# Kernel tuning notes

Measured on AMD Instinct MI355X. Metric: run time of the kernel, lower is better.

## Reference

```python
import jax, jax.numpy as jnp
import numpy as np

B, D = 8192, 128
TEMP = 0.07
EPS = 1e-12  # F.normalize default eps (clamp on norm)


def _l2norm(x):
    n = jnp.sqrt(jnp.sum(x * x, axis=1, keepdims=True))
    return x / jnp.maximum(n, EPS)


def setup_inputs() -> dict:
    key = jax.random.key(0)
    k1, k2, k3, k4 = jax.random.split(key, 4)
    return {
        "feat_fv": jax.random.normal(k1, (B, D), dtype=jnp.float32),
        "feat_fi": jax.random.normal(k2, (B, D), dtype=jnp.float32),
        "feat_v": jax.random.normal(k3, (B, D), dtype=jnp.float32),
        "feat_i": jax.random.normal(k4, (B, D), dtype=jnp.float32),
    }


def reference(feat_fv, feat_fi, feat_v, feat_i):
    fv = _l2norm(feat_fv)
    fi = _l2norm(feat_fi)
    v = _l2norm(feat_v)
    vi = _l2norm(feat_i)

    # positive logits: per-sample dot products [B]
    pos_v = jnp.sum(fv * v, axis=1)
    pos_i = jnp.sum(fi * vi, axis=1)
    use_v = pos_v >= pos_i                      # branch condition per row
    pos = jnp.where(use_v, pos_v, pos_i)        # [B]

    # full pairwise dot products, branch-select per row
    Sv = jnp.einsum('bd,kd->bk', fv, v)         # [B, B]
    Si = jnp.einsum('bd,kd->bk', fi, vi)        # [B, B]
    S = jnp.where(use_v[:, None], Sv, Si)       # [B, B]

    n = S.shape[0]
    diag = jnp.eye(n, dtype=bool)
    # negatives exclude the positive (diagonal) entry -> mask to -inf
    neg_logits = jnp.where(diag, -jnp.inf, S / TEMP)  # [B, B]

    # cross-entropy with target class 0 (the positive), reduction='none':
    # loss_b = logsumexp([pos/T, negs/T]) - pos/T
    lse = jnp.logaddexp(pos / TEMP, jax.scipy.special.logsumexp(neg_logits, axis=1))
    return lse - pos / TEMP
```

## Files before the change

kernel.cpp:

```cpp
#include <hip/hip_runtime.h>
#include <math.h>

#define Bsz 8192
#define Dd  128
#define BM  64
#define NSLICE 16
#define NTILE  (512 / NSLICE / 4)
#define ROT2(x) ((((x) << 2) | ((x) >> 4)) & 63)

typedef __attribute__((ext_vector_type(8))) short short8;
typedef __attribute__((ext_vector_type(4))) float float4v;

static constexpr float INV_T = 1.0f / 0.07f;
static constexpr float K1 =  20.60992915555662f;
static constexpr float K2 = -20.60992915555662f;
static constexpr float SCALE     = 1099511627776.0f;
static constexpr float INV_SCALE = 1.0f / 1099511627776.0f;
#define CNT_SHIFT 55
#define NCONTRIB  (NSLICE * 4)
#define SUM_MASK  ((1ULL << CNT_SHIFT) - 1ULL)

static __device__ inline unsigned pack_bf16(float x, float y) {
    union { float f; unsigned u; } a, b;
    a.f = x; b.f = y;
    unsigned ra = a.u + 0x7FFF + ((a.u >> 16) & 1);
    unsigned rb = b.u + 0x7FFF + ((b.u >> 16) & 1);
    return (ra >> 16) | (rb & 0xFFFF0000u);
}

__global__ void init_kernel(unsigned long long* __restrict__ cnt) {
    if (threadIdx.x == 0) cnt[0] = 0ull;
}

__global__ __launch_bounds__(1024) void prep_kernel(
    const float4* __restrict__ fv4, const float4* __restrict__ fi4,
    const float4* __restrict__ v4,  const float4* __restrict__ vi4,
    unsigned* __restrict__ Xb, uint2* __restrict__ Yf0, uint2* __restrict__ Yf1,
    float* __restrict__ posArr, int* __restrict__ origArr, int* __restrict__ flagArr,
    unsigned long long* __restrict__ lAcc64, unsigned long long* __restrict__ cnt)
{
    __shared__ unsigned sT0[32 * 66];
    __shared__ unsigned sT1[32 * 66];
    __shared__ int sFlagL[32];
    __shared__ int sRank[32];
    __shared__ unsigned sBase[2];

    const int t    = threadIdx.x;
    const int wave = t >> 6;
    const int lane = t & 63;
    const int half = lane >> 5;
    const int c    = lane & 31;
    const int rl   = wave * 2 + half;
    const int b    = blockIdx.x * 32 + rl;
    const int src  = b * 32 + c;

    const float4 afv = fv4[src];
    const float4 afi = fi4[src];
    const float4 av  = v4[src];
    const float4 avi = vi4[src];

    float nfv = afv.x*afv.x + afv.y*afv.y + afv.z*afv.z + afv.w*afv.w;
    float nfi = afi.x*afi.x + afi.y*afi.y + afi.z*afi.z + afi.w*afi.w;
    float nv  = av.x*av.x   + av.y*av.y   + av.z*av.z   + av.w*av.w;
    float nvi = avi.x*avi.x + avi.y*avi.y + avi.z*avi.z + avi.w*avi.w;
    float dv  = afv.x*av.x  + afv.y*av.y  + afv.z*av.z  + afv.w*av.w;
    float di  = afi.x*avi.x + afi.y*avi.y + afi.z*avi.z + afi.w*avi.w;

    #pragma unroll
    for (int m = 1; m < 32; m <<= 1) {
        nfv += __shfl_xor(nfv, m);
        nfi += __shfl_xor(nfi, m);
        nv  += __shfl_xor(nv,  m);
        nvi += __shfl_xor(nvi, m);
        dv  += __shfl_xor(dv,  m);
        di  += __shfl_xor(di,  m);
    }

    const float rnfv = 1.0f / fmaxf(sqrtf(nfv), 1e-12f);
    const float rnfi = 1.0f / fmaxf(sqrtf(nfi), 1e-12f);
    const float rnv  = 1.0f / fmaxf(sqrtf(nv ), 1e-12f);
    const float rnvi = 1.0f / fmaxf(sqrtf(nvi), 1e-12f);

    const float pos_v = dv * rnfv * rnv;
    const float pos_i = di * rnfi * rnvi;
    const bool useV = (pos_v >= pos_i);
    const float pos = useV ? pos_v : pos_i;

    uint2 w0y = make_uint2(pack_bf16(av.x  * rnv,  av.y  * rnv),
                           pack_bf16(av.z  * rnv,  av.w  * rnv));
    uint2 w1y = make_uint2(pack_bf16(avi.x * rnvi, avi.y * rnvi),
                           pack_bf16(avi.z * rnvi, avi.w * rnvi));
    *(uint2*)&sT0[rl * 66 + c * 2] = w0y;
    *(uint2*)&sT1[rl * 66 + c * 2] = w1y;
    if (c == 0) sFlagL[rl] = useV ? 0 : 1;
    __syncthreads();

    if (t < 64) {
        const int f = (lane < 32) ? sFlagL[lane] : 2;
        const unsigned long long m0 = __ballot(f == 0);
        const unsigned long long m1 = __ballot(f == 1);
        if (lane == 0) {
            const unsigned long long add =
                (unsigned long long)__popcll(m0) | ((unsigned long long)__popcll(m1) << 32);
            const unsigned long long ret = atomicAdd(cnt, add);
            sBase[0] = (unsigned)(ret & 0xffffffffull);
            sBase[1] = (unsigned)(ret >> 32);
        }
        if (lane < 32) {
            const unsigned long long below = (1ull << lane) - 1ull;
            sRank[lane] = (f == 0) ? (int)__popcll(m0 & below) : (int)__popcll(m1 & below);
        }
    }

    {
        const int tl = t >> 9;
        const int kc = (t >> 7) & 3;
        const int lp = (t >> 1) & 63;
        const int w0 = (t & 1) * 2;
        const int row = tl * 16 + (lp & 15);
        const int s   = kc * 16 + (lp >> 4) * 4 + w0;
        Yf0[blockIdx.x * 1024 + t] = *(const uint2*)&sT0[row * 66 + s];
        Yf1[blockIdx.x * 1024 + t] = *(const uint2*)&sT1[row * 66 + s];
    }
    __syncthreads();

    const int f  = sFlagL[rl];
    const int rk = sRank[rl];
    const int p  = (f == 0) ? (int)(sBase[0] + rk) : (Bsz - 1 - (int)(sBase[1] + rk));

    const float sc = useV ? rnfv : rnfi;
    const float x0 = useV ? afv.x : afi.x;
    const float x1 = useV ? afv.y : afi.y;
    const float x2 = useV ? afv.z : afi.z;
    const float x3 = useV ? afv.w : afi.w;
    ((uint2*)Xb)[p * 32 + c] = make_uint2(pack_bf16(x0 * sc, x1 * sc),
                                          pack_bf16(x2 * sc, x3 * sc));

    if (c == 0) {
        posArr[p]  = pos;
        origArr[p] = b;
        flagArr[p] = f;
        lAcc64[p]  = 0ull;
    }
}

__global__ __launch_bounds__(256, 4) void main_kernel(
    const unsigned short* __restrict__ Xb,
    const uint4* __restrict__ Yf0q, const uint4* __restrict__ Yf1q,
    const int* __restrict__ flagArr, unsigned long long* __restrict__ lAcc64,
    const float* __restrict__ posArr, const int* __restrict__ origArr,
    float* __restrict__ out)
{
    __shared__ uint4 sXf[1024];
    __shared__ int sFlag[BM];
    __shared__ int sHas[2];

    const int t    = threadIdx.x;
    const int wave = t >> 6;
    const int lane = t & 63;
    const int quad = lane >> 4;
    const int mrow = lane & 15;
    const int slice = blockIdx.x & (NSLICE - 1);
    const int p0    = (blockIdx.x >> 4) * BM;

    if (t < 2) sHas[t] = 0;
    __syncthreads();
    if (t < BM) {
        const int f = flagArr[p0 + t];
        sFlag[t] = f;
        atomicOr(&sHas[f], 1);
    }

    #pragma unroll
    for (int it = 0; it < 4; ++it) {
        const int i = t + it * 256;
        const int row = i >> 4, ch = i & 15;
        const uint4 val = ((const uint4*)Xb)[(p0 + row) * 16 + ch];
        const int blk16 = (row >> 4) * 4 + (ch >> 2);
        const int slot  = (ch & 3) * 16 + (row & 15);
        sXf[blk16 * 64 + ROT2(slot)] = val;
    }
    __syncthreads();

    short8 afr[4][4];
    #pragma unroll
    for (int rt = 0; rt < 4; ++rt)
        #pragma unroll
        for (int kc = 0; kc < 4; ++kc)
            afr[rt][kc] = *(const short8*)&sXf[(rt * 4 + kc) * 64 + ROT2(lane)];

    const int g0 = slice * (NTILE * 4) + wave * NTILE;

    for (int phase = 0; phase < 2; ++phase) {
        if (!sHas[phase]) continue;
        const uint4* __restrict__ yb = (phase ? Yf1q : Yf0q) + (size_t)g0 * 256 + lane;

        float rowsum[4][4] = {};

        short8 b0 = *(const short8*)&yb[0];
        short8 b1 = *(const short8*)&yb[64];
        short8 b2 = *(const short8*)&yb[128];
        short8 b3 = *(const short8*)&yb[192];

        #pragma unroll 1
        for (int jt = 0; jt < NTILE; ++jt) {
            float4v acc[4] = {};
            #pragma unroll
            for (int rt = 0; rt < 4; ++rt)
                acc[rt] = __builtin_amdgcn_mfma_f32_16x16x32_bf16(afr[rt][0], b0, acc[rt], 0, 0, 0);
            #pragma unroll
            for (int rt = 0; rt < 4; ++rt)
                acc[rt] = __builtin_amdgcn_mfma_f32_16x16x32_bf16(afr[rt][1], b1, acc[rt], 0, 0, 0);
            if (jt < NTILE - 1) {
                b0 = *(const short8*)&yb[256];
                b1 = *(const short8*)&yb[320];
            }
            #pragma unroll
            for (int rt = 0; rt < 4; ++rt)
                acc[rt] = __builtin_amdgcn_mfma_f32_16x16x32_bf16(afr[rt][2], b2, acc[rt], 0, 0, 0);
            #pragma unroll
            for (int rt = 0; rt < 4; ++rt)
                acc[rt] = __builtin_amdgcn_mfma_f32_16x16x32_bf16(afr[rt][3], b3, acc[rt], 0, 0, 0);
            if (jt < NTILE - 1) {
                b2 = *(const short8*)&yb[384];
                b3 = *(const short8*)&yb[448];
            }
            yb += 256;

            #pragma unroll
            for (int rt = 0; rt < 4; ++rt)
                #pragma unroll
                for (int r = 0; r < 4; ++r)
                    rowsum[rt][r] += exp2f(fmaf(acc[rt][r], K1, K2));
        }

        #pragma unroll
        for (int m = 1; m < 16; m <<= 1)
            #pragma unroll
            for (int rt = 0; rt < 4; ++rt)
                #pragma unroll
                for (int r = 0; r < 4; ++r)
                    rowsum[rt][r] += __shfl_xor(rowsum[rt][r], m);

        if (mrow == 0) {
            #pragma unroll
            for (int rt = 0; rt < 4; ++rt)
                #pragma unroll
                for (int r = 0; r < 4; ++r) {
                    const int row = rt * 16 + quad * 4 + r;
                    if (sFlag[row] == phase) {
                        const unsigned long long add =
                            (unsigned long long)(rowsum[rt][r] * SCALE)
                            | (1ULL << CNT_SHIFT);
                        const unsigned long long ret =
                            atomicAdd(&lAcc64[p0 + row], add);
                        if ((ret >> CNT_SHIFT) == NCONTRIB - 1) {
                            const unsigned long long tot = (ret + add) & SUM_MASK;
                            const float s = (float)tot * INV_SCALE;
                            out[origArr[p0 + row]] =
                                logf(s) + INV_T - posArr[p0 + row] * INV_T;
                        }
                    }
                }
        }
    }
}

extern "C" void kernel_launch(void* const* d_in, const int* in_sizes, int n_in,
                              void* d_out, int out_size, void* d_ws, size_t ws_size,
                              hipStream_t stream)
{
    const float4* fv = (const float4*)d_in[0];
    const float4* fi = (const float4*)d_in[1];
    const float4* v  = (const float4*)d_in[2];
    const float4* vi = (const float4*)d_in[3];
    float* out = (float*)d_out;

    unsigned short* Xb  = (unsigned short*)d_ws;
    unsigned short* Yf0 = Xb  + Bsz * Dd;
    unsigned short* Yf1 = Yf0 + Bsz * Dd;
    float* posArr = (float*)(Yf1 + Bsz * Dd);
    unsigned long long* lAcc64 =
        (unsigned long long*)(posArr + Bsz);
    int*  origArr = (int*)(lAcc64 + Bsz);
    int*  flagArr = origArr + Bsz;
    unsigned long long* cnt = (unsigned long long*)(flagArr + Bsz);

    hipLaunchKernelGGL(init_kernel, dim3(1), dim3(64), 0, stream, cnt);
    hipLaunchKernelGGL(prep_kernel, dim3(Bsz / 32), dim3(1024), 0, stream,
                       fv, fi, v, vi, (unsigned*)Xb, (uint2*)Yf0, (uint2*)Yf1,
                       posArr, origArr, flagArr, lAcc64, cnt);
    hipLaunchKernelGGL(main_kernel, dim3((Bsz / BM) * NSLICE), dim3(256), 0, stream,
                       Xb, (const uint4*)Yf0, (const uint4*)Yf1, flagArr, lAcc64,
                       posArr, origArr, out);
}
```

Before: 130.9 us.

## Software-pipeline exp with MFMA via double accumulators, halve slices, drop LDS staging

The tile loop now keeps two accumulator sets, so the exp2 row-sum work for the previous tile is interleaved with the MFMAs for the current tile. The aim is to hide transcendental latency behind matrix ops. A fragments are now loaded directly from global memory in MFMA layout instead of being staged through rotated shared memory, which removes one barrier and the LDS traffic. Flag presence is computed with wave ballots instead of shared atomics. NSLICE drops from 16 to 8, which doubles the tiles per wave and halves the number of blocks and atomic contributions per row, at the cost of less parallelism and more registers.

```diff
diff --git a/kernel.cpp b/kernel.cpp
--- a/kernel.cpp
+++ b/kernel.cpp
@@ -4,9 +4,8 @@
 #define Bsz 8192
 #define Dd  128
 #define BM  64
-#define NSLICE 16
+#define NSLICE 8
 #define NTILE  (512 / NSLICE / 4)
-#define ROT2(x) ((((x) << 2) | ((x) >> 4)) & 63)
 
 typedef __attribute__((ext_vector_type(8))) short short8;
 typedef __attribute__((ext_vector_type(4))) float float4v;
@@ -151,7 +150,6 @@
     const float* __restrict__ posArr, const int* __restrict__ origArr,
     float* __restrict__ out)
 {
-    __shared__ uint4 sXf[1024];
     __shared__ int sFlag[BM];
     __shared__ int sHas[2];
 
@@ -161,78 +159,79 @@
     const int quad = lane >> 4;
     const int mrow = lane & 15;
     const int slice = blockIdx.x & (NSLICE - 1);
-    const int p0    = (blockIdx.x >> 4) * BM;
-
-    if (t < 2) sHas[t] = 0;
-    __syncthreads();
-    if (t < BM) {
-        const int f = flagArr[p0 + t];
-        sFlag[t] = f;
-        atomicOr(&sHas[f], 1);
-    }
-
-    #pragma unroll
-    for (int it = 0; it < 4; ++it) {
-        const int i = t + it * 256;
-        const int row = i >> 4, ch = i & 15;
-        const uint4 val = ((const uint4*)Xb)[(p0 + row) * 16 + ch];
-        const int blk16 = (row >> 4) * 4 + (ch >> 2);
-        const int slot  = (ch & 3) * 16 + (row & 15);
-        sXf[blk16 * 64 + ROT2(slot)] = val;
-    }
-    __syncthreads();
+    const int p0    = (blockIdx.x >> 3) * BM;
 
     short8 afr[4][4];
     #pragma unroll
     for (int rt = 0; rt < 4; ++rt)
         #pragma unroll
         for (int kc = 0; kc < 4; ++kc)
-            afr[rt][kc] = *(const short8*)&sXf[(rt * 4 + kc) * 64 + ROT2(lane)];
+            afr[rt][kc] = *(const short8*)&Xb[(size_t)(p0 + rt * 16 + mrow) * 128
+                                              + kc * 32 + quad * 8];
+
+    if (t < 64) {
+        const int f = flagArr[p0 + t];
+        sFlag[t] = f;
+        const unsigned long long m0 = __ballot(f == 0);
+        const unsigned long long m1 = __ballot(f == 1);
+        if (t == 0) { sHas[0] = (m0 != 0ull); sHas[1] = (m1 != 0ull); }
+    }
+    __syncthreads();
 
     const int g0 = slice * (NTILE * 4) + wave * NTILE;
+
+#define MFMA4(ACC, KC, BB)                                                         \
+    _Pragma("unroll")                                                              \
+    for (int rt = 0; rt < 4; ++rt)                                                 \
+        ACC[rt] = __builtin_amdgcn_mfma_f32_16x16x32_bf16(afr[rt][KC], BB, ACC[rt], 0, 0, 0);
+
+#define EXPQ(P, RT)                                                                \
+    _Pragma("unroll")                                                              \
+    for (int r = 0; r < 4; ++r)                                                    \
+        rowsum[RT][r] += exp2f(fmaf(P[RT][r], K1, K2));
+
+#define STEP(ACC, PACC, PF) do {                                                   \
+        ACC[0] = (float4v){0.f,0.f,0.f,0.f}; ACC[1] = (float4v){0.f,0.f,0.f,0.f};  \
+        ACC[2] = (float4v){0.f,0.f,0.f,0.f}; ACC[3] = (float4v){0.f,0.f,0.f,0.f};  \
+        MFMA4(ACC, 0, b0); MFMA4(ACC, 1, b1);                                      \
+        EXPQ(PACC, 0); EXPQ(PACC, 1);                                              \
+        if (PF) { b0 = *(const short8*)&yb[256]; b1 = *(const short8*)&yb[320]; }  \
+        MFMA4(ACC, 2, b2); MFMA4(ACC, 3, b3);                                      \
+        EXPQ(PACC, 2); EXPQ(PACC, 3);                                              \
+        if (PF) { b2 = *(const short8*)&yb[384]; b3 = *(const short8*)&yb[448]; }  \
+        yb += 256;                                                                 \
+    } while (0)
+
+#define STEP0(ACC, PF) do {                                                        \
+        ACC[0] = (float4v){0.f,0.f,0.f,0.f}; ACC[1] = (float4v){0.f,0.f,0.f,0.f};  \
+        ACC[2] = (float4v){0.f,0.f,0.f,0.f}; ACC[3] = (float4v){0.f,0.f,0.f,0.f};  \
+        MFMA4(ACC, 0, b0); MFMA4(ACC, 1, b1);                                      \
+        if (PF) { b0 = *(const short8*)&yb[256]; b1 = *(const short8*)&yb[320]; }  \
+        MFMA4(ACC, 2, b2); MFMA4(ACC, 3, b3);                                      \
+        if (PF) { b2 = *(const short8*)&yb[384]; b3 = *(const short8*)&yb[448]; }  \
+        yb += 256;                                                                 \
+    } while (0)
 
     for (int phase = 0; phase < 2; ++phase) {
         if (!sHas[phase]) continue;
         const uint4* __restrict__ yb = (phase ? Yf1q : Yf0q) + (size_t)g0 * 256 + lane;
 
         float rowsum[4][4] = {};
+        float4v accA[4], accB[4];
 
         short8 b0 = *(const short8*)&yb[0];
         short8 b1 = *(const short8*)&yb[64];
         short8 b2 = *(const short8*)&yb[128];
         short8 b3 = *(const short8*)&yb[192];
 
+        STEP0(accA, 1);
         #pragma unroll 1
-        for (int jt = 0; jt < NTILE; ++jt) {
-            float4v acc[4] = {};
-            #pragma unroll
-            for (int rt = 0; rt < 4; ++rt)
-                acc[rt] = __builtin_amdgcn_mfma_f32_16x16x32_bf16(afr[rt][0], b0, acc[rt], 0, 0, 0);
-            #pragma unroll
-            for (int rt = 0; rt < 4; ++rt)
-                acc[rt] = __builtin_amdgcn_mfma_f32_16x16x32_bf16(afr[rt][1], b1, acc[rt], 0, 0, 0);
-            if (jt < NTILE - 1) {
-                b0 = *(const short8*)&yb[256];
-                b1 = *(const short8*)&yb[320];
-            }
-            #pragma unroll
-            for (int rt = 0; rt < 4; ++rt)
-                acc[rt] = __builtin_amdgcn_mfma_f32_16x16x32_bf16(afr[rt][2], b2, acc[rt], 0, 0, 0);
-            #pragma unroll
-            for (int rt = 0; rt < 4; ++rt)
-                acc[rt] = __builtin_amdgcn_mfma_f32_16x16x32_bf16(afr[rt][3], b3, acc[rt], 0, 0, 0);
-            if (jt < NTILE - 1) {
-                b2 = *(const short8*)&yb[384];
-                b3 = *(const short8*)&yb[448];
-            }
-            yb += 256;
-
-            #pragma unroll
-            for (int rt = 0; rt < 4; ++rt)
-                #pragma unroll
-                for (int r = 0; r < 4; ++r)
-                    rowsum[rt][r] += exp2f(fmaf(acc[rt][r], K1, K2));
-        }
+        for (int i = 0; i < 7; ++i) {
+            STEP(accB, accA, 1);
+            STEP(accA, accB, 1);
+        }
+        STEP(accB, accA, 0);
+        EXPQ(accB, 0); EXPQ(accB, 1); EXPQ(accB, 2); EXPQ(accB, 3);
 
         #pragma unroll
         for (int m = 1; m < 16; m <<= 1)
@@ -264,6 +263,10 @@
                 }
         }
     }
+#undef STEP0
+#undef STEP
+#undef EXPQ
+#undef MFMA4
 }
 
 extern "C" void kernel_launch(void* const* d_in, const int* in_sizes, int n_in,
```

New measurement: 180.6 us. 38.0% more time.

## Split block into 2x2 wave grid with per-wave 32-row A fragments from global

Applied to the files above, without the earlier changes.

Waves now form a 2x2 grid in each block: each wave holds A fragments for 32 rows (instead of all 64) and covers a larger column range, with 8 slices per row block instead of 16. The A fragments are loaded straight from global memory, which removes the shared-memory staging buffer and its swizzle. The row-presence flags are now computed with a ballot rather than shared-memory atomics. Together these cut register pressure and LDS use and halve the number of atomic contributions per row, but each wave issues only two independent MFMA chains per step, which leaves less instruction-level parallelism to hide MFMA latency.

```diff
diff --git a/kernel.cpp b/kernel.cpp
--- a/kernel.cpp
+++ b/kernel.cpp
@@ -4,9 +4,8 @@
 #define Bsz 8192
 #define Dd  128
 #define BM  64
-#define NSLICE 16
-#define NTILE  (512 / NSLICE / 4)
-#define ROT2(x) ((((x) << 2) | ((x) >> 4)) & 63)
+#define NSLICE 8
+#define NTILE  (512 / NSLICE / 2)
 
 typedef __attribute__((ext_vector_type(8))) short short8;
 typedef __attribute__((ext_vector_type(4))) float float4v;
@@ -17,7 +16,7 @@
 static constexpr float SCALE     = 1099511627776.0f;
 static constexpr float INV_SCALE = 1.0f / 1099511627776.0f;
 #define CNT_SHIFT 55
-#define NCONTRIB  (NSLICE * 4)
+#define NCONTRIB  (NSLICE * 2)
 #define SUM_MASK  ((1ULL << CNT_SHIFT) - 1ULL)
 
 static __device__ inline unsigned pack_bf16(float x, float y) {
@@ -151,51 +150,43 @@
     const float* __restrict__ posArr, const int* __restrict__ origArr,
     float* __restrict__ out)
 {
-    __shared__ uint4 sXf[1024];
     __shared__ int sFlag[BM];
     __shared__ int sHas[2];
 
     const int t    = threadIdx.x;
     const int wave = t >> 6;
+    const int wr   = wave >> 1;
+    const int wc   = wave & 1;
     const int lane = t & 63;
     const int quad = lane >> 4;
     const int mrow = lane & 15;
     const int slice = blockIdx.x & (NSLICE - 1);
-    const int p0    = (blockIdx.x >> 4) * BM;
-
-    if (t < 2) sHas[t] = 0;
-    __syncthreads();
-    if (t < BM) {
+    const int p0    = (blockIdx.x >> 3) * BM;
+
+    short8 afr[2][4];
+    #pragma unroll
+    for (int rt = 0; rt < 2; ++rt)
+        #pragma unroll
+        for (int kc = 0; kc < 4; ++kc)
+            afr[rt][kc] = *(const short8*)&Xb[(size_t)(p0 + wr * 32 + rt * 16 + mrow) * 128
+                                              + kc * 32 + quad * 8];
+
+    if (t < 64) {
         const int f = flagArr[p0 + t];
         sFlag[t] = f;
-        atomicOr(&sHas[f], 1);
-    }
-
-    #pragma unroll
-    for (int it = 0; it < 4; ++it) {
-        const int i = t + it * 256;
-        const int row = i >> 4, ch = i & 15;
-        const uint4 val = ((const uint4*)Xb)[(p0 + row) * 16 + ch];
-        const int blk16 = (row >> 4) * 4 + (ch >> 2);
-        const int slot  = (ch & 3) * 16 + (row & 15);
-        sXf[blk16 * 64 + ROT2(slot)] = val;
+        const unsigned long long m0 = __ballot(f == 0);
+        const unsigned long long m1 = __ballot(f == 1);
+        if (t == 0) { sHas[0] = (m0 != 0ull); sHas[1] = (m1 != 0ull); }
     }
     __syncthreads();
 
-    short8 afr[4][4];
-    #pragma unroll
-    for (int rt = 0; rt < 4; ++rt)
-        #pragma unroll
-        for (int kc = 0; kc < 4; ++kc)
-            afr[rt][kc] = *(const short8*)&sXf[(rt * 4 + kc) * 64 + ROT2(lane)];
-
-    const int g0 = slice * (NTILE * 4) + wave * NTILE;
+    const int g0 = slice * 64 + wc * NTILE;
 
     for (int phase = 0; phase < 2; ++phase) {
         if (!sHas[phase]) continue;
         const uint4* __restrict__ yb = (phase ? Yf1q : Yf0q) + (size_t)g0 * 256 + lane;
 
-        float rowsum[4][4] = {};
+        float rowsum[2][4] = {};
 
         short8 b0 = *(const short8*)&yb[0];
         short8 b1 = *(const short8*)&yb[64];
@@ -204,23 +195,20 @@
 
         #pragma unroll 1
         for (int jt = 0; jt < NTILE; ++jt) {
-            float4v acc[4] = {};
-            #pragma unroll
-            for (int rt = 0; rt < 4; ++rt)
-                acc[rt] = __builtin_amdgcn_mfma_f32_16x16x32_bf16(afr[rt][0], b0, acc[rt], 0, 0, 0);
-            #pragma unroll
-            for (int rt = 0; rt < 4; ++rt)
-                acc[rt] = __builtin_amdgcn_mfma_f32_16x16x32_bf16(afr[rt][1], b1, acc[rt], 0, 0, 0);
+            float4v acc0 = {0.f, 0.f, 0.f, 0.f};
+            float4v acc1 = {0.f, 0.f, 0.f, 0.f};
+            acc0 = __builtin_amdgcn_mfma_f32_16x16x32_bf16(afr[0][0], b0, acc0, 0, 0, 0);
+            acc1 = __builtin_amdgcn_mfma_f32_16x16x32_bf16(afr[1][0], b0, acc1, 0, 0, 0);
+            acc0 = __builtin_amdgcn_mfma_f32_16x16x32_bf16(afr[0][1], b1, acc0, 0, 0, 0);
+            acc1 = __builtin_amdgcn_mfma_f32_16x16x32_bf16(afr[1][1], b1, acc1, 0, 0, 0);
             if (jt < NTILE - 1) {
                 b0 = *(const short8*)&yb[256];
                 b1 = *(const short8*)&yb[320];
             }
-            #pragma unroll
-            for (int rt = 0; rt < 4; ++rt)
-                acc[rt] = __builtin_amdgcn_mfma_f32_16x16x32_bf16(afr[rt][2], b2, acc[rt], 0, 0, 0);
-            #pragma unroll
-            for (int rt = 0; rt < 4; ++rt)
-                acc[rt] = __builtin_amdgcn_mfma_f32_16x16x32_bf16(afr[rt][3], b3, acc[rt], 0, 0, 0);
+            acc0 = __builtin_amdgcn_mfma_f32_16x16x32_bf16(afr[0][2], b2, acc0, 0, 0, 0);
+            acc1 = __builtin_amdgcn_mfma_f32_16x16x32_bf16(afr[1][2], b2, acc1, 0, 0, 0);
+            acc0 = __builtin_amdgcn_mfma_f32_16x16x32_bf16(afr[0][3], b3, acc0, 0, 0, 0);
+            acc1 = __builtin_amdgcn_mfma_f32_16x16x32_bf16(afr[1][3], b3, acc1, 0, 0, 0);
             if (jt < NTILE - 1) {
                 b2 = *(const short8*)&yb[384];
                 b3 = *(const short8*)&yb[448];
@@ -228,26 +216,27 @@
             yb += 256;
 
             #pragma unroll
-            for (int rt = 0; rt < 4; ++rt)
-                #pragma unroll
-                for (int r = 0; r < 4; ++r)
-                    rowsum[rt][r] += exp2f(fmaf(acc[rt][r], K1, K2));
+            for (int r = 0; r < 4; ++r)
+                rowsum[0][r] += exp2f(fmaf(acc0[r], K1, K2));
+            #pragma unroll
+            for (int r = 0; r < 4; ++r)
+                rowsum[1][r] += exp2f(fmaf(acc1[r], K1, K2));
         }
 
         #pragma unroll
         for (int m = 1; m < 16; m <<= 1)
             #pragma unroll
-            for (int rt = 0; rt < 4; ++rt)
+            for (int rt = 0; rt < 2; ++rt)
                 #pragma unroll
                 for (int r = 0; r < 4; ++r)
                     rowsum[rt][r] += __shfl_xor(rowsum[rt][r], m);
 
         if (mrow == 0) {
             #pragma unroll
-            for (int rt = 0; rt < 4; ++rt)
+            for (int rt = 0; rt < 2; ++rt)
                 #pragma unroll
                 for (int r = 0; r < 4; ++r) {
-                    const int row = rt * 16 + quad * 4 + r;
+                    const int row = wr * 32 + rt * 16 + quad * 4 + r;
                     if (sFlag[row] == phase) {
                         const unsigned long long add =
                             (unsigned long long)(rowsum[rt][r] * SCALE)
```

Measured after the change: 119.7 us. -8.5%, faster.
